# Kernel optimization log

Hardware: AMD Instinct MI355X
Metric: run time of the kernel (lower is better)

The kernel has to match this reference:

```python
import jax, jax.numpy as jnp
import numpy as np

B, IN_NUM, IN_DIM = 64, 4096, 8
NUM_CAPS, DIM_CAPS, ROUTINGS = 32, 16, 3
EPS = 1e-7  # keras.backend.epsilon()


def squash(v, axis=-1):
    # squash(s) = ||s||^2/(1+||s||^2) * s/||s||
    s2 = jnp.sum(v * v, axis=axis, keepdims=True)
    return (s2 / (1.0 + s2)) * v / jnp.sqrt(s2 + EPS)


def setup_inputs() -> dict:
    key = jax.random.key(0)
    k1, k2 = jax.random.split(key)
    inputs = jax.random.normal(k1, (B, IN_NUM, IN_DIM), dtype=jnp.float32)
    # kernel: [num_capsule, input_num_capsule, dim_capsule, input_dim_capsule]
    W = jax.random.normal(k2, (NUM_CAPS, IN_NUM, DIM_CAPS, IN_DIM), dtype=jnp.float32) * 0.05
    return {"inputs": inputs, "W": W}


def reference(inputs, W):
    # prediction vectors u_hat[b,c,n,j] = sum_i W[c,n,j,i] * x[b,n,i]
    hat = jnp.einsum('bni,cnji->bcnj', inputs, W)  # [B, C, N, D]
    b = jnp.zeros(hat.shape[:3], hat.dtype)        # routing logits [B, C, N]
    out = None
    for i in range(ROUTINGS):
        c = jax.nn.softmax(b, axis=1)              # couple over output capsules
        out = squash(jnp.einsum('bcn,bcnj->bcj', c, hat))  # [B, C, D]
        if i < ROUTINGS - 1:
            b = b + jnp.einsum('bcj,bcnj->bcn', out, hat)  # agreement update
    return out
```

## Files before the change

kernel.cpp:

```cpp
#include <hip/hip_runtime.h>
#include <math.h>


typedef __fp16 h2 __attribute__((ext_vector_type(2)));
typedef __fp16 half4 __attribute__((ext_vector_type(4)));
typedef float f32x16 __attribute__((ext_vector_type(16)));

union U2 { h2 h; unsigned u; };

__device__ __forceinline__ float fdot2(h2 a, h2 b, float c) {
    return __builtin_amdgcn_fdot2(a, b, c, false);
}
__device__ __forceinline__ h2 uash2(unsigned u) { U2 t; t.u = u; return t.h; }


template <int NPB>
__global__ __launch_bounds__(512, 4) void pass0_kernel(
    const float* __restrict__ W,
    const float* __restrict__ x,
    ushort* __restrict__ Wh,
    ushort* __restrict__ xh,
    unsigned* __restrict__ partial)
{
    constexpr int NB = 4096 / NPB;
    const int bid = blockIdx.x;
    const int half = bid / NB, nblk = bid % NB;
    const int n0 = nblk * NPB;
    const int t = threadIdx.x, l = t & 63, w = t >> 6;
    const int bl = l & 31, hi = l >> 5;
    const int cj = half * 256 + w * 32 + bl;

    __shared__ __align__(16) ushort xs[NPB * 512];
    __shared__ unsigned sep[8192];

    #pragma unroll
    for (int rep = 0; rep < NPB / 4; ++rep) {
        const int idx = t + rep * 512;
        const int b = idx / (2 * NPB), f4 = idx % (2 * NPB);
        const int nl = f4 >> 1, isl = f4 & 1;
        float4 v = *reinterpret_cast<const float4*>(
            x + (size_t)b * 32768 + (size_t)n0 * 8 + f4 * 4);
        half4 h;
        h[0] = (__fp16)v.x; h[1] = (__fp16)v.y; h[2] = (__fp16)v.z; h[3] = (__fp16)v.w;
        const int slot = (nl * 128 + b * 2 + isl) ^ ((nl & 7) << 1) ^ ((b >> 3) & 3);
        *reinterpret_cast<half4*>(xs + slot * 4) = h;
    }
    __syncthreads();

    if (half == 0) {
        #pragma unroll
        for (int rep = 0; rep < NPB / 4; ++rep) {
            const int u = t + rep * 512;
            const int nl = u >> 7, b = (u >> 1) & 63, isl = u & 1;
            const int slot = (nl * 128 + b * 2 + isl) ^ ((nl & 7) << 1) ^ ((b >> 3) & 3);
            half4 h = *reinterpret_cast<const half4*>(xs + slot * 4);
            *reinterpret_cast<half4*>(xh + (size_t)n0 * 512 + u * 4) = h;
        }
    }

    const float* wb = W + (size_t)(cj >> 4) * 524288 + (size_t)n0 * 128 + (cj & 15) * 8 + hi * 4;
    ushort* whp = Wh + ((size_t)n0 * 512 + cj) * 8 + hi * 4;

    f32x16 acc0 = {}, acc1 = {};
    float4 wv = *reinterpret_cast<const float4*>(wb);
    #pragma unroll 1
    for (int s = 0; s < NPB; ++s) {
        float4 wvn;
        if (s < NPB - 1)
            wvn = *reinterpret_cast<const float4*>(wb + (s + 1) * 128);
        const int sw = ((s & 7) << 1) ^ ((bl >> 3) & 3);
        const int slot0 = (s * 128 + bl * 2 + hi) ^ sw;
        const int slot1 = (s * 128 + bl * 2 + 64 + hi) ^ sw;
        half4 b0 = *reinterpret_cast<const half4*>(xs + slot0 * 4);
        half4 b1 = *reinterpret_cast<const half4*>(xs + slot1 * 4);
        half4 a;
        a[0] = (__fp16)wv.x; a[1] = (__fp16)wv.y; a[2] = (__fp16)wv.z; a[3] = (__fp16)wv.w;
        *reinterpret_cast<half4*>(whp + (size_t)s * 4096) = a;
        acc0 = __builtin_amdgcn_mfma_f32_32x32x8f16(a, b0, acc0, 0, 0, 0);
        acc1 = __builtin_amdgcn_mfma_f32_32x32x8f16(a, b1, acc1, 0, 0, 0);
        wv = wvn;
    }
    #pragma unroll
    for (int r = 0; r < 16; ++r) { acc0[r] *= 0.03125f; acc1[r] *= 0.03125f; }

    #pragma unroll
    for (int hb = 0; hb < 2; ++hb) {
        #pragma unroll
        for (int q = 0; q < 8; ++q) {
            const float e0 = hb ? acc1[2 * q] : acc0[2 * q];
            const float e1 = hb ? acc1[2 * q + 1] : acc0[2 * q + 1];
            U2 u; u.h = __builtin_amdgcn_cvt_pkrtz(e0, e1);
            const int cjp = w * 16 + 4 * (q >> 1) + (q & 1) + 2 * hi;
            const int bb = bl + 32 * hb;
            sep[bb * 128 + (cjp ^ bb)] = u.u;
        }
    }
    __syncthreads();
    #pragma unroll
    for (int u2 = 0; u2 < 16; ++u2) {
        const int idx = t + u2 * 512;
        const int ub = idx >> 7, ucjp = idx & 127;
        partial[(size_t)((ub >> 5) * NB + nblk) * 8192 + (ub & 31) * 256 + half * 128 + ucjp]
            = sep[ub * 128 + (ucjp ^ ub)];
    }
}


template <int NPB>
__global__ __launch_bounds__(512, 4) void pass12_kernel(
    const ushort* __restrict__ Wh,
    const ushort* __restrict__ xh,
    const ushort* __restrict__ OcumG,
    unsigned* __restrict__ partial)
{
    constexpr int NB = 4096 / NPB;
    const int bid = blockIdx.x;
    const int bt = bid / NB, nblk = bid % NB;
    const int n0 = nblk * NPB;
    const int t = threadIdx.x, l = t & 63, w = t >> 6;
    const int bl = l & 31, hi = l >> 5;
    const int b = bt * 32 + bl;

    __shared__ __align__(16) float pd[2][32][12];
    __shared__ unsigned sep[8192];

    const int cj0 = w * 64 + bl, cj1 = cj0 + 32;
    const ushort* xb = xh + ((size_t)n0 * 64 + b) * 8 + hi * 4;
    const ushort* whp0 = Wh + ((size_t)n0 * 512 + cj0) * 8 + hi * 4;
    const ushort* whp1 = Wh + ((size_t)n0 * 512 + cj1) * 8 + hi * 4;

    h2 oc[2][8];
    {
        const unsigned* og = reinterpret_cast<const unsigned*>(OcumG);
        #pragma unroll
        for (int mt = 0; mt < 2; ++mt) {
            const int cA = 4 * w + 2 * mt;
            const unsigned idx = (unsigned)b * 256 + cA * 8 + hi * 2;
            oc[mt][0] = uash2(og[idx]);      oc[mt][1] = uash2(og[idx + 1]);
            oc[mt][2] = uash2(og[idx + 4]);  oc[mt][3] = uash2(og[idx + 5]);
            oc[mt][4] = uash2(og[idx + 8]);  oc[mt][5] = uash2(og[idx + 9]);
            oc[mt][6] = uash2(og[idx + 12]); oc[mt][7] = uash2(og[idx + 13]);
        }
    }

    f32x16 zero = {};
    f32x16 acc0 = {}, acc1 = {};

    half4 a0 = *reinterpret_cast<const half4*>(whp0);
    half4 a1 = *reinterpret_cast<const half4*>(whp1);
    half4 bf = *reinterpret_cast<const half4*>(xb);
    #pragma unroll 1
    for (int s = 0; s < NPB; ++s) {
        half4 a0n, a1n, bfn;
        if (s < NPB - 1) {
            a0n = *reinterpret_cast<const half4*>(whp0 + (size_t)(s + 1) * 4096);
            a1n = *reinterpret_cast<const half4*>(whp1 + (size_t)(s + 1) * 4096);
            bfn = *reinterpret_cast<const half4*>(xb + (size_t)(s + 1) * 512);
        }
        f32x16 d0 = __builtin_amdgcn_mfma_f32_32x32x8f16(a0, bf, zero, 0, 0, 0);
        f32x16 d1 = __builtin_amdgcn_mfma_f32_32x32x8f16(a1, bf, zero, 0, 0, 0);
        h2 h0[8], h1[8];
        #pragma unroll
        for (int q = 0; q < 8; ++q) {
            h0[q] = __builtin_amdgcn_cvt_pkrtz(d0[2 * q], d0[2 * q + 1]);
            h1[q] = __builtin_amdgcn_cvt_pkrtz(d1[2 * q], d1[2 * q + 1]);
        }
        float pA0 = fdot2(h0[3], oc[0][3], fdot2(h0[2], oc[0][2], fdot2(h0[1], oc[0][1], fdot2(h0[0], oc[0][0], 0.f))));
        float pB0 = fdot2(h0[7], oc[0][7], fdot2(h0[6], oc[0][6], fdot2(h0[5], oc[0][5], fdot2(h0[4], oc[0][4], 0.f))));
        float pA1 = fdot2(h1[3], oc[1][3], fdot2(h1[2], oc[1][2], fdot2(h1[1], oc[1][1], fdot2(h1[0], oc[1][0], 0.f))));
        float pB1 = fdot2(h1[7], oc[1][7], fdot2(h1[6], oc[1][6], fdot2(h1[5], oc[1][5], fdot2(h1[4], oc[1][4], 0.f))));
        pA0 += __shfl_xor(pA0, 32, 64);
        pB0 += __shfl_xor(pB0, 32, 64);
        pA1 += __shfl_xor(pA1, 32, 64);
        pB1 += __shfl_xor(pB1, 32, 64);
        float eA0 = __expf(pA0), eB0 = __expf(pB0), eA1 = __expf(pA1), eB1 = __expf(pB1);
        const int buf = s & 1;
        if (l < 32) pd[buf][bl][w] = eA0 + eB0 + eA1 + eB1;
        __syncthreads();
        const float4 q0 = *reinterpret_cast<const float4*>(&pd[buf][bl][0]);
        const float4 q1 = *reinterpret_cast<const float4*>(&pd[buf][bl][4]);
        const float rd = __builtin_amdgcn_rcpf(q0.x + q0.y + q0.z + q0.w +
                                               q1.x + q1.y + q1.z + q1.w);
        const float cA0 = eA0 * rd, cB0 = eB0 * rd, cA1 = eA1 * rd, cB1 = eB1 * rd;
        #pragma unroll
        for (int r = 0; r < 8; ++r)  { acc0[r] += d0[r] * cA0; acc1[r] += d1[r] * cA1; }
        #pragma unroll
        for (int r = 8; r < 16; ++r) { acc0[r] += d0[r] * cB0; acc1[r] += d1[r] * cB1; }
        a0 = a0n; a1 = a1n; bf = bfn;
    }

    __syncthreads();
    #pragma unroll
    for (int mt = 0; mt < 2; ++mt) {
        #pragma unroll
        for (int q = 0; q < 8; ++q) {
            const float e0 = mt ? acc1[2 * q] : acc0[2 * q];
            const float e1 = mt ? acc1[2 * q + 1] : acc0[2 * q + 1];
            U2 u; u.h = __builtin_amdgcn_cvt_pkrtz(e0, e1);
            const int cjp = w * 32 + mt * 16 + 4 * (q >> 1) + (q & 1) + 2 * hi;
            sep[bl * 256 + (cjp ^ bl)] = u.u;
        }
    }
    __syncthreads();
    const unsigned gbase = (unsigned)bid * 8192;
    #pragma unroll
    for (int u2 = 0; u2 < 16; ++u2) {
        const int idx = t + u2 * 512;
        const int ubl = idx >> 8, ucjp = idx & 255;
        partial[gbase + idx] = sep[ubl * 256 + (ucjp ^ ubl)];
    }
}


template <int NB>
__global__ __launch_bounds__(256) void reduce_squash(const unsigned* __restrict__ partial32,
                                                     ushort* __restrict__ OcumG,
                                                     float* __restrict__ out,
                                                     int passIdx) {
    const int gtid = blockIdx.x * 256 + threadIdx.x;
    const int oid = gtid >> 2, sub = gtid & 3;
    const int b = oid >> 8, cjp = oid & 255;
    const int bt = b >> 5, bl = b & 31;
    const unsigned base = (unsigned)bt * (unsigned)NB * 8192u + (unsigned)bl * 256u + (unsigned)cjp;
    float sx = 0.f, sy = 0.f;
    #pragma unroll 8
    for (int i = 0; i < NB / 4; ++i) {
        U2 v; v.u = partial32[base + (unsigned)(sub + 4 * i) * 8192u];
        sx += (float)v.h.x;
        sy += (float)v.h.y;
    }
    sx += __shfl_xor(sx, 1, 64); sy += __shfl_xor(sy, 1, 64);
    sx += __shfl_xor(sx, 2, 64); sy += __shfl_xor(sy, 2, 64);
    float s2 = sx * sx + sy * sy;
    s2 += __shfl_xor(s2, 4, 64);
    s2 += __shfl_xor(s2, 8, 64);
    s2 += __shfl_xor(s2, 16, 64);
    float scale = (s2 / (1.f + s2)) / sqrtf(s2 + 1e-7f);
    float o0 = scale * sx, o1 = scale * sy;

    if (sub == 0) {
        unsigned* ocp = reinterpret_cast<unsigned*>(OcumG) + b * 256 + cjp;
        float a0 = o0, a1 = o1;
        if (passIdx) {
            U2 old; old.u = *ocp;
            a0 += (float)old.h.x;
            a1 += (float)old.h.y;
        }
        U2 nw; nw.h = __builtin_amdgcn_cvt_pkrtz(a0, a1);
        *ocp = nw.u;
        if (passIdx == 2) {
            out[b * 512 + cjp * 2] = o0;
            out[b * 512 + cjp * 2 + 1] = o1;
        }
    }
}


extern "C" void kernel_launch(void* const* d_in, const int* in_sizes, int n_in,
                              void* d_out, int out_size, void* d_ws, size_t ws_size,
                              hipStream_t stream) {
    const float* x = (const float*)d_in[0];
    const float* W = (const float*)d_in[1];
    float* out = (float*)d_out;

    char* ws = (char*)d_ws;
    ushort* Wh = (ushort*)ws;
    const size_t MiB = 1024 * 1024;

    if (ws_size >= 52 * MiB + 65536) {
        unsigned* partialU = (unsigned*)(ws + 32 * MiB);
        ushort* xh = (ushort*)(ws + 48 * MiB);
        ushort* OcumG = (ushort*)(ws + 52 * MiB);
        pass0_kernel<16><<<512, 512, 0, stream>>>(W, x, Wh, xh, partialU);
        reduce_squash<256><<<256, 256, 0, stream>>>(partialU, OcumG, out, 0);
        pass12_kernel<16><<<512, 512, 0, stream>>>(Wh, xh, OcumG, partialU);
        reduce_squash<256><<<256, 256, 0, stream>>>(partialU, OcumG, out, 1);
        pass12_kernel<16><<<512, 512, 0, stream>>>(Wh, xh, OcumG, partialU);
        reduce_squash<256><<<256, 256, 0, stream>>>(partialU, OcumG, out, 2);
    } else {
        unsigned* partialU = (unsigned*)(ws + 32 * MiB);
        ushort* xh = (ushort*)(ws + 40 * MiB);
        ushort* OcumG = (ushort*)(ws + 44 * MiB);
        pass0_kernel<32><<<256, 512, 0, stream>>>(W, x, Wh, xh, partialU);
        reduce_squash<128><<<256, 256, 0, stream>>>(partialU, OcumG, out, 0);
        pass12_kernel<32><<<256, 512, 0, stream>>>(Wh, xh, OcumG, partialU);
        reduce_squash<128><<<256, 256, 0, stream>>>(partialU, OcumG, out, 1);
        pass12_kernel<32><<<256, 512, 0, stream>>>(Wh, xh, OcumG, partialU);
        reduce_squash<128><<<256, 256, 0, stream>>>(partialU, OcumG, out, 2);
    }
}
```

Baseline: 170.8 us.

## Process two input capsules per barrier and accumulate routing sums in packed fp16

The pass-1/2 loop now handles two n-steps per iteration, so the shared-memory softmax-denominator exchange and its __syncthreads run half as often. The register prefetch is doubled to match. The weighted accumulation of prediction vectors changes from fp32 FMAs to packed fp16 multiply-adds on the already-converted halves, which cuts VALU work and register pressure. In exchange, accumulating in fp16 over many steps adds rounding error and overflow risk, and the extra live registers may hurt occupancy. NPB is assumed to be even.

```diff
diff --git a/kernel.cpp b/kernel.cpp
--- a/kernel.cpp
+++ b/kernel.cpp
@@ -121,7 +121,7 @@
     const int bl = l & 31, hi = l >> 5;
     const int b = bt * 32 + bl;
 
-    __shared__ __align__(16) float pd[2][32][12];
+    __shared__ __align__(16) float pd[2][2][32][12];
     __shared__ unsigned sep[8192];
 
     const int cj0 = w * 64 + bl, cj1 = cj0 + 32;
@@ -144,59 +144,124 @@
     }
 
     f32x16 zero = {};
-    f32x16 acc0 = {}, acc1 = {};
-
-    half4 a0 = *reinterpret_cast<const half4*>(whp0);
-    half4 a1 = *reinterpret_cast<const half4*>(whp1);
-    half4 bf = *reinterpret_cast<const half4*>(xb);
+    h2 acc0h[8], acc1h[8];
+    #pragma unroll
+    for (int q = 0; q < 8; ++q) {
+        acc0h[q] = (h2)(__fp16)0.f;
+        acc1h[q] = (h2)(__fp16)0.f;
+    }
+
+    half4 a0A = *reinterpret_cast<const half4*>(whp0);
+    half4 a1A = *reinterpret_cast<const half4*>(whp1);
+    half4 bfA = *reinterpret_cast<const half4*>(xb);
+    half4 a0B = *reinterpret_cast<const half4*>(whp0 + 4096);
+    half4 a1B = *reinterpret_cast<const half4*>(whp1 + 4096);
+    half4 bfB = *reinterpret_cast<const half4*>(xb + 512);
+
     #pragma unroll 1
-    for (int s = 0; s < NPB; ++s) {
-        half4 a0n, a1n, bfn;
-        if (s < NPB - 1) {
-            a0n = *reinterpret_cast<const half4*>(whp0 + (size_t)(s + 1) * 4096);
-            a1n = *reinterpret_cast<const half4*>(whp1 + (size_t)(s + 1) * 4096);
-            bfn = *reinterpret_cast<const half4*>(xb + (size_t)(s + 1) * 512);
-        }
-        f32x16 d0 = __builtin_amdgcn_mfma_f32_32x32x8f16(a0, bf, zero, 0, 0, 0);
-        f32x16 d1 = __builtin_amdgcn_mfma_f32_32x32x8f16(a1, bf, zero, 0, 0, 0);
-        h2 h0[8], h1[8];
+    for (int p = 0; p < NPB / 2; ++p) {
+        half4 a0An, a1An, bfAn, a0Bn, a1Bn, bfBn;
+        if (p < NPB / 2 - 1) {
+            const int sA = 2 * p + 2, sB = 2 * p + 3;
+            a0An = *reinterpret_cast<const half4*>(whp0 + (size_t)sA * 4096);
+            a1An = *reinterpret_cast<const half4*>(whp1 + (size_t)sA * 4096);
+            bfAn = *reinterpret_cast<const half4*>(xb + (size_t)sA * 512);
+            a0Bn = *reinterpret_cast<const half4*>(whp0 + (size_t)sB * 4096);
+            a1Bn = *reinterpret_cast<const half4*>(whp1 + (size_t)sB * 4096);
+            bfBn = *reinterpret_cast<const half4*>(xb + (size_t)sB * 512);
+        }
+        h2 hA0[8], hA1[8];
+        {
+            f32x16 d0 = __builtin_amdgcn_mfma_f32_32x32x8f16(a0A, bfA, zero, 0, 0, 0);
+            f32x16 d1 = __builtin_amdgcn_mfma_f32_32x32x8f16(a1A, bfA, zero, 0, 0, 0);
+            #pragma unroll
+            for (int q = 0; q < 8; ++q) {
+                hA0[q] = __builtin_amdgcn_cvt_pkrtz(d0[2 * q], d0[2 * q + 1]);
+                hA1[q] = __builtin_amdgcn_cvt_pkrtz(d1[2 * q], d1[2 * q + 1]);
+            }
+        }
+        float pA0_A = fdot2(hA0[3], oc[0][3], fdot2(hA0[2], oc[0][2], fdot2(hA0[1], oc[0][1], fdot2(hA0[0], oc[0][0], 0.f))));
+        float pB0_A = fdot2(hA0[7], oc[0][7], fdot2(hA0[6], oc[0][6], fdot2(hA0[5], oc[0][5], fdot2(hA0[4], oc[0][4], 0.f))));
+        float pA1_A = fdot2(hA1[3], oc[1][3], fdot2(hA1[2], oc[1][2], fdot2(hA1[1], oc[1][1], fdot2(hA1[0], oc[1][0], 0.f))));
+        float pB1_A = fdot2(hA1[7], oc[1][7], fdot2(hA1[6], oc[1][6], fdot2(hA1[5], oc[1][5], fdot2(hA1[4], oc[1][4], 0.f))));
+        h2 hB0[8], hB1[8];
+        {
+            f32x16 d0 = __builtin_amdgcn_mfma_f32_32x32x8f16(a0B, bfB, zero, 0, 0, 0);
+            f32x16 d1 = __builtin_amdgcn_mfma_f32_32x32x8f16(a1B, bfB, zero, 0, 0, 0);
+            #pragma unroll
+            for (int q = 0; q < 8; ++q) {
+                hB0[q] = __builtin_amdgcn_cvt_pkrtz(d0[2 * q], d0[2 * q + 1]);
+                hB1[q] = __builtin_amdgcn_cvt_pkrtz(d1[2 * q], d1[2 * q + 1]);
+            }
+        }
+        float pA0_B = fdot2(hB0[3], oc[0][3], fdot2(hB0[2], oc[0][2], fdot2(hB0[1], oc[0][1], fdot2(hB0[0], oc[0][0], 0.f))));
+        float pB0_B = fdot2(hB0[7], oc[0][7], fdot2(hB0[6], oc[0][6], fdot2(hB0[5], oc[0][5], fdot2(hB0[4], oc[0][4], 0.f))));
+        float pA1_B = fdot2(hB1[3], oc[1][3], fdot2(hB1[2], oc[1][2], fdot2(hB1[1], oc[1][1], fdot2(hB1[0], oc[1][0], 0.f))));
+        float pB1_B = fdot2(hB1[7], oc[1][7], fdot2(hB1[6], oc[1][6], fdot2(hB1[5], oc[1][5], fdot2(hB1[4], oc[1][4], 0.f))));
+
+        pA0_A += __shfl_xor(pA0_A, 32, 64);
+        pB0_A += __shfl_xor(pB0_A, 32, 64);
+        pA1_A += __shfl_xor(pA1_A, 32, 64);
+        pB1_A += __shfl_xor(pB1_A, 32, 64);
+        pA0_B += __shfl_xor(pA0_B, 32, 64);
+        pB0_B += __shfl_xor(pB0_B, 32, 64);
+        pA1_B += __shfl_xor(pA1_B, 32, 64);
+        pB1_B += __shfl_xor(pB1_B, 32, 64);
+
+        float eA0_A = __expf(pA0_A), eB0_A = __expf(pB0_A);
+        float eA1_A = __expf(pA1_A), eB1_A = __expf(pB1_A);
+        float eA0_B = __expf(pA0_B), eB0_B = __expf(pB0_B);
+        float eA1_B = __expf(pA1_B), eB1_B = __expf(pB1_B);
+
+        const int buf = p & 1;
+        if (l < 32) {
+            pd[buf][0][bl][w] = eA0_A + eB0_A + eA1_A + eB1_A;
+            pd[buf][1][bl][w] = eA0_B + eB0_B + eA1_B + eB1_B;
+        }
+        __syncthreads();
+        const float4 qa0 = *reinterpret_cast<const float4*>(&pd[buf][0][bl][0]);
+        const float4 qa1 = *reinterpret_cast<const float4*>(&pd[buf][0][bl][4]);
+        const float4 qb0 = *reinterpret_cast<const float4*>(&pd[buf][1][bl][0]);
+        const float4 qb1 = *reinterpret_cast<const float4*>(&pd[buf][1][bl][4]);
+        const float rdA = __builtin_amdgcn_rcpf(qa0.x + qa0.y + qa0.z + qa0.w +
+                                                qa1.x + qa1.y + qa1.z + qa1.w);
+        const float rdB = __builtin_amdgcn_rcpf(qb0.x + qb0.y + qb0.z + qb0.w +
+                                                qb1.x + qb1.y + qb1.z + qb1.w);
+
+        h2 c0A, c1A, c0B, c1B, c2A, c3A, c2B, c3B;
+        c0A.x = (__fp16)(eA0_A * rdA); c0A.y = c0A.x;
+        c1A.x = (__fp16)(eB0_A * rdA); c1A.y = c1A.x;
+        c2A.x = (__fp16)(eA1_A * rdA); c2A.y = c2A.x;
+        c3A.x = (__fp16)(eB1_A * rdA); c3A.y = c3A.x;
+        c0B.x = (__fp16)(eA0_B * rdB); c0B.y = c0B.x;
+        c1B.x = (__fp16)(eB0_B * rdB); c1B.y = c1B.x;
+        c2B.x = (__fp16)(eA1_B * rdB); c2B.y = c2B.x;
+        c3B.x = (__fp16)(eB1_B * rdB); c3B.y = c3B.x;
+
+        #pragma unroll
+        for (int q = 0; q < 4; ++q) {
+            acc0h[q] = hA0[q] * c0A + acc0h[q];
+            acc0h[q + 4] = hA0[q + 4] * c1A + acc0h[q + 4];
+            acc1h[q] = hA1[q] * c2A + acc1h[q];
+            acc1h[q + 4] = hA1[q + 4] * c3A + acc1h[q + 4];
+        }
+        #pragma unroll
+        for (int q = 0; q < 4; ++q) {
+            acc0h[q] = hB0[q] * c0B + acc0h[q];
+            acc0h[q + 4] = hB0[q + 4] * c1B + acc0h[q + 4];
+            acc1h[q] = hB1[q] * c2B + acc1h[q];
+            acc1h[q + 4] = hB1[q + 4] * c3B + acc1h[q + 4];
+        }
+        a0A = a0An; a1A = a1An; bfA = bfAn;
+        a0B = a0Bn; a1B = a1Bn; bfB = bfBn;
+    }
+
+    __syncthreads();
+    #pragma unroll
+    for (int mt = 0; mt < 2; ++mt) {
         #pragma unroll
         for (int q = 0; q < 8; ++q) {
-            h0[q] = __builtin_amdgcn_cvt_pkrtz(d0[2 * q], d0[2 * q + 1]);
-            h1[q] = __builtin_amdgcn_cvt_pkrtz(d1[2 * q], d1[2 * q + 1]);
-        }
-        float pA0 = fdot2(h0[3], oc[0][3], fdot2(h0[2], oc[0][2], fdot2(h0[1], oc[0][1], fdot2(h0[0], oc[0][0], 0.f))));
-        float pB0 = fdot2(h0[7], oc[0][7], fdot2(h0[6], oc[0][6], fdot2(h0[5], oc[0][5], fdot2(h0[4], oc[0][4], 0.f))));
-        float pA1 = fdot2(h1[3], oc[1][3], fdot2(h1[2], oc[1][2], fdot2(h1[1], oc[1][1], fdot2(h1[0], oc[1][0], 0.f))));
-        float pB1 = fdot2(h1[7], oc[1][7], fdot2(h1[6], oc[1][6], fdot2(h1[5], oc[1][5], fdot2(h1[4], oc[1][4], 0.f))));
-        pA0 += __shfl_xor(pA0, 32, 64);
-        pB0 += __shfl_xor(pB0, 32, 64);
-        pA1 += __shfl_xor(pA1, 32, 64);
-        pB1 += __shfl_xor(pB1, 32, 64);
-        float eA0 = __expf(pA0), eB0 = __expf(pB0), eA1 = __expf(pA1), eB1 = __expf(pB1);
-        const int buf = s & 1;
-        if (l < 32) pd[buf][bl][w] = eA0 + eB0 + eA1 + eB1;
-        __syncthreads();
-        const float4 q0 = *reinterpret_cast<const float4*>(&pd[buf][bl][0]);
-        const float4 q1 = *reinterpret_cast<const float4*>(&pd[buf][bl][4]);
-        const float rd = __builtin_amdgcn_rcpf(q0.x + q0.y + q0.z + q0.w +
-                                               q1.x + q1.y + q1.z + q1.w);
-        const float cA0 = eA0 * rd, cB0 = eB0 * rd, cA1 = eA1 * rd, cB1 = eB1 * rd;
-        #pragma unroll
-        for (int r = 0; r < 8; ++r)  { acc0[r] += d0[r] * cA0; acc1[r] += d1[r] * cA1; }
-        #pragma unroll
-        for (int r = 8; r < 16; ++r) { acc0[r] += d0[r] * cB0; acc1[r] += d1[r] * cB1; }
-        a0 = a0n; a1 = a1n; bf = bfn;
-    }
-
-    __syncthreads();
-    #pragma unroll
-    for (int mt = 0; mt < 2; ++mt) {
-        #pragma unroll
-        for (int q = 0; q < 8; ++q) {
-            const float e0 = mt ? acc1[2 * q] : acc0[2 * q];
-            const float e1 = mt ? acc1[2 * q + 1] : acc0[2 * q + 1];
-            U2 u; u.h = __builtin_amdgcn_cvt_pkrtz(e0, e1);
+            U2 u; u.h = mt ? acc1h[q] : acc0h[q];
             const int cjp = w * 32 + mt * 16 + 4 * (q >> 1) + (q & 1) + 2 * hi;
             sep[bl * 256 + (cjp ^ bl)] = u.u;
         }
```

New measurement: 167.6 us. Within noise of the previous version (-1.9%).
